# Optimization experiments

Hardware: AMD Instinct MI355X
Metric: run time of the kernel (lower is better)

## Reference

```python
import jax, jax.numpy as jnp
import numpy as np

V, D, E, S, L = 32000, 1024, 2048, 128, 4  # vocab, d_model, e=expansion*d, d_head, n_layers
B, T = 2, 2048


def _layernorm(x, g, b, eps=1e-5):
    mu = jnp.mean(x, axis=-1, keepdims=True)
    var = jnp.var(x, axis=-1, keepdims=True)
    return (x - mu) * jax.lax.rsqrt(var + eps) * g + b


def _rope_tables(t, dim):
    half = dim // 2
    inv_freq = 1.0 / (10000.0 ** (jnp.arange(0, dim, 2, dtype=jnp.float32) / dim))  # (half,)
    freqs = jnp.arange(t, dtype=jnp.float32)[:, None] * inv_freq[None, :]           # (T, half)
    return jnp.cos(freqs), jnp.sin(freqs)


def _apply_rope(x, cos, sin):
    half = x.shape[-1] // 2
    x1, x2 = x[..., :half], x[..., half:]
    return jnp.concatenate([x1 * cos - x2 * sin, x1 * sin + x2 * cos], axis=-1)


def setup_inputs() -> dict:
    key = jax.random.key(0)
    ks = jax.random.split(key, 12)
    def init(k, shape, fan_in):
        return jax.random.normal(k, shape, jnp.float32) * (fan_in ** -0.5)
    return {
        "tokens": jax.random.randint(ks[0], (B, T), 0, V, dtype=jnp.int64),
        "emb":    init(ks[1], (V, D), D),
        "Wu":     init(ks[2], (L, D, E), D),
        "Wv":     init(ks[3], (L, D, E), D),
        "Wq":     init(ks[4], (L, E, S), E),
        "Wk":     init(ks[5], (L, E, S), E),
        "Wo":     init(ks[6], (L, E, D), E),
        "ln_g":   jnp.ones((L, D), jnp.float32),
        "ln_b":   jnp.zeros((L, D), jnp.float32),
        "lnf_g":  jnp.ones((D,), jnp.float32),
        "lnf_b":  jnp.zeros((D,), jnp.float32),
        "Wlm":    init(ks[7], (D, V), D),
    }


def reference(tokens, emb, Wu, Wv, Wq, Wk, Wo, ln_g, ln_b, lnf_g, lnf_b, Wlm):
    t = tokens.shape[1]
    cos, sin = _rope_tables(t, S)                      # (T, S/2) each
    causal = jnp.tril(jnp.ones((t, t), bool))          # causal mask
    scale = 1.0 / np.sqrt(S)
    x = emb[tokens]                                    # (B, T, D)
    for i in range(L):
        xn = _layernorm(x, ln_g[i], ln_b[i])
        u = jax.nn.silu(xn @ Wu[i])                    # (B, T, E) gate branch
        v = jax.nn.silu(xn @ Wv[i])                    # (B, T, E) value branch
        q = _apply_rope(u @ Wq[i], cos, sin)           # (B, T, S)
        k = _apply_rope(v @ Wk[i], cos, sin)           # (B, T, S)
        attn = jnp.einsum('bts,bus->btu', q, k) * scale   # (B, T, T) single-head
        attn = jnp.where(causal, attn, -1e9)
        attn = jnp.square(jnp.maximum(attn, 0.0))      # relu^2 instead of softmax
        av = jnp.einsum('btu,bue->bte', attn, v)       # (B, T, E)
        x = x + (u * av) @ Wo[i]                       # gated output + residual
    x = _layernorm(x, lnf_g, lnf_b)
    return x @ Wlm                                     # (B, T, V) logits
```

## Files before the change

kernel.cpp:

```cpp
#include <hip/hip_runtime.h>
#include <math.h>


#define Bz 2
#define Tt 2048
#define Dd 1024
#define Ee 2048
#define Ss 128
#define Ll 4
#define Vv 32000
#define BT (Bz * Tt)

typedef __attribute__((ext_vector_type(8))) _Float16 f16x8;
typedef __attribute__((ext_vector_type(4))) _Float16 f16x4;
typedef __attribute__((ext_vector_type(4))) float    f32x4;

__device__ __forceinline__ void load_lds16(const void* g, void* l) {
  __builtin_amdgcn_global_load_lds(
      (const __attribute__((address_space(1))) void*)g,
      (__attribute__((address_space(3))) void*)l, 16, 0, 0);
}

#define FENCE asm volatile("" ::: "memory")
#define BARRIER do { FENCE; __builtin_amdgcn_s_barrier(); FENCE; } while (0)

enum { EPI_F32 = 0, EPI_SILU = 1, EPI_SCORES = 2, EPI_RESID = 3, EPI_GATED = 4 };

__device__ __forceinline__ int xcd_swz(int id, int nwg) {
  int q = nwg >> 3, r = nwg & 7;
  int x = id & 7, o = id >> 3;
  return (x < r ? x * (q + 1) : r * (q + 1) + (x - r) * q) + o;
}

template <int EPI>
__global__ void __launch_bounds__(512) gemm256(
    const _Float16* __restrict__ A, long sA,
    const _Float16* __restrict__ Bt, long sB,
    void* __restrict__ Cp, long sC,
    int M, int N, int K, int lda, int ldb, int ldc) {
  const int bz = blockIdx.z;
  A += (size_t)bz * sA;
  Bt += (size_t)bz * sB;

  const int nbm = M >> 8;
  const int id = xcd_swz(blockIdx.x, gridDim.x);
  const int bm = id % nbm, bn = id / nbm;
  const int row0 = bm << 8, col0 = bn << 8;

  __shared__ __align__(16) char smem[131072];
  _Float16* const Abuf0 = (_Float16*)smem;
  _Float16* const Bbuf0 = (_Float16*)(smem + 65536);

  const int tid = threadIdx.x, lane = tid & 63, w = tid >> 6;
  const int mu = w >> 2, nu = w & 3;
  const int fr = lane & 15, kg = lane >> 4;
  const int srow = (w << 3) + (lane >> 3);
  const int sg = (lane & 7) ^ ((lane >> 3) & 7);
  const _Float16* Asrc = A + (size_t)(row0 + srow) * lda + sg * 8;
  const _Float16* Bsrc = Bt + (size_t)(col0 + srow) * ldb + sg * 8;
  const int gx[2] = { ((kg) ^ (fr & 7)) << 3, ((4 + kg) ^ (fr & 7)) << 3 };

#define ST_A(BUF, KT, Q) load_lds16(Asrc + (size_t)(Q) * 64 * lda + (size_t)(KT) * 64, \
                                    (void*)&Abuf0[(BUF) * 16384 + (Q) * 4096 + (w << 9)])
#define ST_B(BUF, KT, Q) load_lds16(Bsrc + (size_t)(Q) * 64 * ldb + (size_t)(KT) * 64, \
                                    (void*)&Bbuf0[(BUF) * 16384 + (Q) * 4096 + (w << 9)])
#define RD_A(BUF, MH)                                                          \
  { _Pragma("unroll") for (int j = 0; j < 4; ++j)                              \
    _Pragma("unroll") for (int ks = 0; ks < 2; ++ks)                           \
      af[j][ks] = *(const f16x8*)&Abuf0[(BUF) * 16384 +                        \
          (mu * 128 + (MH) * 64 + j * 16 + fr) * 64 + gx[ks]]; }
#define RD_B(BUF, NH, BQ)                                                      \
  { _Pragma("unroll") for (int i = 0; i < 2; ++i)                              \
    _Pragma("unroll") for (int ks = 0; ks < 2; ++ks)                           \
      BQ[i][ks] = *(const f16x8*)&Bbuf0[(BUF) * 16384 +                        \
          (nu * 64 + (NH) * 32 + i * 16 + fr) * 64 + gx[ks]]; }
#define MFMA_Q(MH, NH, BQ)                                                     \
  { _Pragma("unroll") for (int ks = 0; ks < 2; ++ks)                           \
    _Pragma("unroll") for (int j = 0; j < 4; ++j)                              \
    _Pragma("unroll") for (int i = 0; i < 2; ++i)                              \
      acc[(MH) * 4 + j][(NH) * 2 + i] = __builtin_amdgcn_mfma_f32_16x16x32_f16( \
          af[j][ks], BQ[i][ks], acc[(MH) * 4 + j][(NH) * 2 + i], 0, 0, 0); }

  f32x4 acc[8][4];
#pragma unroll
  for (int m = 0; m < 8; ++m)
#pragma unroll
    for (int n = 0; n < 4; ++n)
#pragma unroll
      for (int e = 0; e < 4; ++e) acc[m][n][e] = 0.f;

  f16x8 af[4][2], bfA[2][2], bfB[2][2];

  const int NT = K >> 6;
  ST_B(0, 0, 0); ST_B(0, 0, 1); ST_B(0, 0, 2); ST_B(0, 0, 3);
  ST_A(0, 0, 0); ST_A(0, 0, 1); ST_A(0, 0, 2); ST_A(0, 0, 3);
  asm volatile("s_waitcnt vmcnt(0)" ::: "memory");
  BARRIER;

  for (int t = 0; t < NT; ++t) {
    const int b = t & 1, nb = b ^ 1;
    const int kn = (t + 1 < NT) ? t + 1 : t;
    RD_A(b, 0);
    RD_B(b, 0, bfA);
    RD_B(b, 1, bfB);
    ST_B(nb, kn, 0); ST_B(nb, kn, 1); ST_B(nb, kn, 2); ST_B(nb, kn, 3);
    ST_A(nb, kn, 0); ST_A(nb, kn, 1); ST_A(nb, kn, 2); ST_A(nb, kn, 3);
    asm volatile("s_waitcnt lgkmcnt(4)" ::: "memory");
    __builtin_amdgcn_sched_barrier(0);
    __builtin_amdgcn_s_setprio(1); MFMA_Q(0, 0, bfA); __builtin_amdgcn_s_setprio(0);
    asm volatile("s_waitcnt lgkmcnt(0)" ::: "memory");
    __builtin_amdgcn_sched_barrier(0);
    __builtin_amdgcn_s_setprio(1); MFMA_Q(0, 1, bfB); __builtin_amdgcn_s_setprio(0);
    RD_A(b, 1);
    asm volatile("s_waitcnt lgkmcnt(0)" ::: "memory");
    __builtin_amdgcn_sched_barrier(0);
    __builtin_amdgcn_s_setprio(1); MFMA_Q(1, 0, bfA); MFMA_Q(1, 1, bfB);
    __builtin_amdgcn_s_setprio(0);
    asm volatile("s_waitcnt vmcnt(0)" ::: "memory");
    BARRIER;
  }

  if (EPI == EPI_F32) {
    float* Cb = (float*)Cp + (size_t)bz * sC;
#pragma unroll
    for (int p = 0; p < 2; ++p) {
      __syncthreads();
      if (mu == p) {
#pragma unroll
        for (int m = 0; m < 8; ++m)
#pragma unroll
          for (int n = 0; n < 4; ++n) {
            int rl = m * 16 + (kg << 2);
            int col = nu * 64 + n * 16 + fr;
#pragma unroll
            for (int r = 0; r < 4; ++r) {
              int row = rl + r;
              *(float*)(smem + (row << 10) + ((col << 2) ^ ((row & 7) << 4))) =
                  acc[m][n][r];
            }
          }
      }
      __syncthreads();
#pragma unroll
      for (int j = 0; j < 16; ++j) {
        int row = j * 8 + w;
        f32x4 d = *(const f32x4*)(smem + (row << 10) +
                                  ((lane << 4) ^ ((row & 7) << 4)));
        *(f32x4*)&Cb[(size_t)(row0 + p * 128 + row) * ldc + col0 + (lane << 2)] = d;
      }
    }
  } else {
    _Float16* Ch = (_Float16*)Cp + (size_t)bz * sC;
    __syncthreads();
#pragma unroll
    for (int m = 0; m < 8; ++m)
#pragma unroll
      for (int n = 0; n < 4; ++n) {
        int rl = mu * 128 + m * 16 + (kg << 2);
        int col = nu * 64 + n * 16 + fr;
#pragma unroll
        for (int r = 0; r < 4; ++r) {
          int row = rl + r;
          float v = acc[m][n][r];
          *(_Float16*)(smem + (row << 9) + ((col << 1) ^ ((row & 7) << 4))) =
              (_Float16)(v / (1.f + expf(-v)));
        }
      }
    __syncthreads();
#pragma unroll
    for (int j = 0; j < 16; ++j) {
      int row = j * 16 + w * 2 + (lane >> 5);
      int g = lane & 31;
      f16x8 d = *(const f16x8*)(smem + (row << 9) +
                                ((g << 4) ^ ((row & 7) << 4)));
      *(f16x8*)&Ch[(size_t)(row0 + row) * ldc + col0 + (g << 3)] = d;
    }
  }
#undef ST_A
#undef ST_B
#undef RD_A
#undef RD_B
#undef MFMA_Q
}

#define BM 128
#define BN 128
#define BK 32

template <int EPI>
__global__ void __launch_bounds__(256, 2) gemm_bt(
    const _Float16* __restrict__ A, long sA,
    const _Float16* __restrict__ Bt, long sB,
    void* __restrict__ Cp, long sC,
    int M, int N, int K, int lda, int ldb, int ldc, int causal,
    const _Float16* __restrict__ U) {
  int bm = blockIdx.x, bn = blockIdx.y, bz = blockIdx.z;
  if (EPI == EPI_SCORES && bn > bm) return;
  A += (size_t)bz * sA;
  Bt += (size_t)bz * sB;

  int Keff = K;
  if (causal == 2) {
    int km = (bm + 1) * BM;
    Keff = km < K ? km : K;
  }

  __shared__ __align__(16) _Float16 As[BM * BK];
  __shared__ __align__(16) _Float16 Bs[BN * BK];

  int tid = threadIdx.x;
  int lane = tid & 63, wave = tid >> 6;
  int wr = (wave >> 1) << 6;
  int wc = (wave & 1) << 6;
  int row0 = bm * BM, col0 = bn * BN;
  int fr = lane & 15;
  int kg = lane >> 4;
  int srow = lane >> 2;
  int scol = (lane & 3) << 3;

  f32x4 acc[4][4];
#pragma unroll
  for (int i = 0; i < 4; i++)
#pragma unroll
    for (int j = 0; j < 4; j++)
#pragma unroll
      for (int e = 0; e < 4; e++) acc[i][j][e] = 0.f;

  const f16x8* As8 = (const f16x8*)As;
  const f16x8* Bs8 = (const f16x8*)Bs;

  for (int k0 = 0; k0 < Keff; k0 += BK) {
    __syncthreads();
#pragma unroll
    for (int i = 0; i < 2; i++) {
      int rb = (wave * 2 + i) * 16;
      load_lds16(A + (size_t)(row0 + rb + srow) * lda + k0 + scol,
                 (void*)&As[rb * BK]);
      load_lds16(Bt + (size_t)(col0 + rb + srow) * ldb + k0 + scol,
                 (void*)&Bs[rb * BK]);
    }
    asm volatile("s_waitcnt vmcnt(0)" ::: "memory");
    __syncthreads();

    f16x8 af[4], bf[4];
#pragma unroll
    for (int m = 0; m < 4; m++)
      af[m] = As8[(size_t)(wr + m * 16 + fr) * (BK / 8) + kg];
#pragma unroll
    for (int n = 0; n < 4; n++)
      bf[n] = Bs8[(size_t)(wc + n * 16 + fr) * (BK / 8) + kg];
#pragma unroll
    for (int m = 0; m < 4; m++)
#pragma unroll
      for (int n = 0; n < 4; n++)
        acc[m][n] =
            __builtin_amdgcn_mfma_f32_16x16x32_f16(af[m], bf[n], acc[m][n], 0, 0, 0);
  }

#pragma unroll
  for (int m = 0; m < 4; m++) {
    int gr0 = row0 + wr + m * 16 + (kg << 2);
#pragma unroll
    for (int n = 0; n < 4; n++) {
      int gc = col0 + wc + n * 16 + fr;
#pragma unroll
      for (int r = 0; r < 4; r++) {
        float v = acc[m][n][r];
        size_t ci = (size_t)(gr0 + r) * ldc + gc;
        if (EPI == EPI_F32) {
          ((float*)Cp + (size_t)bz * sC)[ci] = v;
        } else if (EPI == EPI_SILU) {
          ((_Float16*)Cp + (size_t)bz * sC)[ci] =
              (_Float16)(v / (1.f + expf(-v)));
        } else if (EPI == EPI_SCORES) {
          float s = v * 0.08838834764831845f;
          s = fmaxf(s, 0.f);
          s = (gc <= gr0 + r) ? s * s : 0.f;
          ((_Float16*)Cp + (size_t)bz * sC)[ci] = (_Float16)s;
        } else if (EPI == EPI_GATED) {
          const _Float16* Ub = U + (size_t)bz * sC;
          ((_Float16*)Cp + (size_t)bz * sC)[ci] = (_Float16)((float)Ub[ci] * v);
        } else {
          ((float*)Cp)[ci] += v;
        }
      }
    }
  }
}

__global__ void __launch_bounds__(256) ln_kernel(const float* __restrict__ x,
                                                 const float* __restrict__ g,
                                                 const float* __restrict__ b,
                                                 _Float16* __restrict__ out) {
  int row = blockIdx.x, tid = threadIdx.x;
  float4 v = ((const float4*)(x + (size_t)row * Dd))[tid];
  float s = v.x + v.y + v.z + v.w;
  float q = v.x * v.x + v.y * v.y + v.z * v.z + v.w * v.w;
#pragma unroll
  for (int off = 32; off > 0; off >>= 1) {
    s += __shfl_down(s, off, 64);
    q += __shfl_down(q, off, 64);
  }
  __shared__ float ss[4], sq[4];
  int lane = tid & 63, wv = tid >> 6;
  if (lane == 0) { ss[wv] = s; sq[wv] = q; }
  __syncthreads();
  s = ss[0] + ss[1] + ss[2] + ss[3];
  q = sq[0] + sq[1] + sq[2] + sq[3];
  float mu = s * (1.f / Dd);
  float var = q * (1.f / Dd) - mu * mu;
  float rs = rsqrtf(var + 1e-5f);
  float4 gg = ((const float4*)g)[tid];
  float4 bb = ((const float4*)b)[tid];
  f16x4 o;
  o[0] = (_Float16)((v.x - mu) * rs * gg.x + bb.x);
  o[1] = (_Float16)((v.y - mu) * rs * gg.y + bb.y);
  o[2] = (_Float16)((v.z - mu) * rs * gg.z + bb.z);
  o[3] = (_Float16)((v.w - mu) * rs * gg.w + bb.w);
  ((f16x4*)(out + (size_t)row * Dd))[tid] = o;
}

__global__ void embed_kernel(const int* __restrict__ toks,
                             const float* __restrict__ emb,
                             float* __restrict__ x) {
  int row = blockIdx.x, tid = threadIdx.x;
  long t = toks[row];
  ((float4*)(x + (size_t)row * Dd))[tid] =
      ((const float4*)(emb + (size_t)t * Dd))[tid];
}

__global__ void rope_table_kernel(float* __restrict__ cosT,
                                  float* __restrict__ sinT) {
  int idx = blockIdx.x * 256 + threadIdx.x;
  int t = idx >> 6, i = idx & 63;
  float inv = powf(10000.f, (float)(2 * i) * (-1.f / 128.f));
  float a = (float)t * inv;
  cosT[idx] = cosf(a);
  sinT[idx] = sinf(a);
}

__global__ void rope_kernel(const float* __restrict__ pre,
                            _Float16* __restrict__ o16,
                            const float* __restrict__ cosT,
                            const float* __restrict__ sinT) {
  int row = blockIdx.x * 4 + threadIdx.y;
  int i = threadIdx.x;
  int z = blockIdx.y;
  const float* p = pre + (size_t)z * BT * Ss + (size_t)row * Ss;
  _Float16* o = o16 + (size_t)z * BT * Ss + (size_t)row * Ss;
  int t = row & (Tt - 1);
  float c = cosT[t * 64 + i], sn = sinT[t * 64 + i];
  float x1 = p[i], x2 = p[i + 64];
  o[i] = (_Float16)(x1 * c - x2 * sn);
  o[i + 64] = (_Float16)(x1 * sn + x2 * c);
}

template <typename TIn>
__global__ void transconv_kernel(const TIn* __restrict__ in,
                                 _Float16* __restrict__ out, int R, int C,
                                 long s_in, long s_out) {
  __shared__ float tile[64][65];
  in += (size_t)blockIdx.z * s_in;
  out += (size_t)blockIdx.z * s_out;
  int r0 = blockIdx.y * 64, c0 = blockIdx.x * 64;
  int tx = threadIdx.x & 63, ty = threadIdx.x >> 6;
#pragma unroll
  for (int p = 0; p < 16; p++) {
    int r = p * 4 + ty;
    tile[r][tx] = (float)in[(size_t)(r0 + r) * C + c0 + tx];
  }
  __syncthreads();
#pragma unroll
  for (int p = 0; p < 16; p++) {
    int r = p * 4 + ty;
    out[(size_t)(c0 + r) * R + r0 + tx] = (_Float16)tile[tx][r];
  }
}

extern "C" void kernel_launch(void* const* d_in, const int* in_sizes, int n_in,
                              void* d_out, int out_size, void* d_ws,
                              size_t ws_size, hipStream_t stream) {
  const int*   tokens = (const int*)d_in[0];
  const float* emb    = (const float*)d_in[1];
  const float* Wu     = (const float*)d_in[2];
  const float* Wv     = (const float*)d_in[3];
  const float* Wq     = (const float*)d_in[4];
  const float* Wk     = (const float*)d_in[5];
  const float* Wo     = (const float*)d_in[6];
  const float* ln_g   = (const float*)d_in[7];
  const float* ln_b   = (const float*)d_in[8];
  const float* lnf_g  = (const float*)d_in[9];
  const float* lnf_b  = (const float*)d_in[10];
  const float* Wlm    = (const float*)d_in[11];
  float* out = (float*)d_out;
  (void)in_sizes; (void)n_in; (void)out_size;

  char* wsp = (char*)d_ws;
  size_t off = 0;
  auto alloc = [&](size_t bytes) -> void* {
    void* p = wsp + off;
    off = (off + bytes + 255) & ~(size_t)255;
    return p;
  };

  float*    x     = (float*)alloc((size_t)BT * Dd * 4);
  _Float16* xn    = (_Float16*)alloc((size_t)BT * Dd * 2);
  _Float16* uvh   = (_Float16*)alloc((size_t)2 * BT * Ee * 2);
  _Float16* vT    = (_Float16*)alloc((size_t)Bz * Ee * Tt * 2);
  float*    qkpre = (float*)alloc((size_t)2 * BT * Ss * 4);
  _Float16* qkh   = (_Float16*)alloc((size_t)2 * BT * Ss * 2);
  _Float16* attn  = (_Float16*)alloc((size_t)Bz * Tt * Tt * 2);
  _Float16* gh    = (_Float16*)alloc((size_t)BT * Ee * 2);
  float*    cosT  = (float*)alloc((size_t)Tt * 64 * 4);
  float*    sinT  = (float*)alloc((size_t)Tt * 64 * 4);
  _Float16* WuvT  = (_Float16*)alloc((size_t)2 * Ll * Ee * Dd * 2);
  _Float16* WqkT  = (_Float16*)alloc((size_t)2 * Ll * Ss * Ee * 2);
  _Float16* WoT   = (_Float16*)alloc((size_t)Ll * Dd * Ee * 2);
  _Float16* WlmT  = (_Float16*)alloc((size_t)Vv * Dd * 2);
  if (off > ws_size) return;

  transconv_kernel<float><<<dim3(Ee / 64, Dd / 64, Ll), 256, 0, stream>>>(
      Wu, WuvT, Dd, Ee, (long)Dd * Ee, (long)Ee * Dd);
  transconv_kernel<float><<<dim3(Ee / 64, Dd / 64, Ll), 256, 0, stream>>>(
      Wv, WuvT + (size_t)Ll * Ee * Dd, Dd, Ee, (long)Dd * Ee, (long)Ee * Dd);
  transconv_kernel<float><<<dim3(Ss / 64, Ee / 64, Ll), 256, 0, stream>>>(
      Wq, WqkT, Ee, Ss, (long)Ee * Ss, (long)Ss * Ee);
  transconv_kernel<float><<<dim3(Ss / 64, Ee / 64, Ll), 256, 0, stream>>>(
      Wk, WqkT + (size_t)Ll * Ss * Ee, Ee, Ss, (long)Ee * Ss, (long)Ss * Ee);
  transconv_kernel<float><<<dim3(Dd / 64, Ee / 64, Ll), 256, 0, stream>>>(
      Wo, WoT, Ee, Dd, (long)Ee * Dd, (long)Dd * Ee);
  transconv_kernel<float><<<dim3(Vv / 64, Dd / 64, 1), 256, 0, stream>>>(
      Wlm, WlmT, Dd, Vv, 0, 0);

  rope_table_kernel<<<(Tt * 64) / 256, 256, 0, stream>>>(cosT, sinT);
  embed_kernel<<<BT, 256, 0, stream>>>(tokens, emb, x);

  for (int l = 0; l < Ll; l++) {
    ln_kernel<<<BT, 256, 0, stream>>>(x, ln_g + (size_t)l * Dd,
                                      ln_b + (size_t)l * Dd, xn);
    gemm256<EPI_SILU><<<dim3((BT / 256) * (Ee / 256), 1, 2), 512, 0, stream>>>(
        xn, 0, WuvT + (size_t)l * Ee * Dd, (long)Ll * Ee * Dd, (void*)uvh,
        (long)BT * Ee, BT, Ee, Dd, Dd, Dd, Ee);
    gemm_bt<EPI_F32><<<dim3(BT / BM, Ss / BN, 2), 256, 0, stream>>>(
        uvh, (long)BT * Ee, WqkT + (size_t)l * Ss * Ee, (long)Ll * Ss * Ee,
        (void*)qkpre, (long)BT * Ss, BT, Ss, Ee, Ee, Ee, Ss, 0, nullptr);
    rope_kernel<<<dim3(BT / 4, 2), dim3(64, 4), 0, stream>>>(qkpre, qkh, cosT,
                                                             sinT);
    transconv_kernel<_Float16><<<dim3(Ee / 64, Tt / 64, Bz), 256, 0, stream>>>(
        uvh + (size_t)BT * Ee, vT, Tt, Ee, (long)Tt * Ee, (long)Ee * Tt);
    gemm_bt<EPI_SCORES><<<dim3(Tt / BM, Tt / BN, Bz), 256, 0, stream>>>(
        qkh, (long)Tt * Ss, qkh + (size_t)BT * Ss, (long)Tt * Ss, (void*)attn,
        (long)Tt * Tt, Tt, Tt, Ss, Ss, Ss, Tt, 0, nullptr);
    gemm_bt<EPI_GATED><<<dim3(Tt / BM, Ee / BN, Bz), 256, 0, stream>>>(
        attn, (long)Tt * Tt, vT, (long)Ee * Tt, (void*)gh, (long)Tt * Ee, Tt,
        Ee, Tt, Tt, Tt, Ee, 2, uvh);
    gemm_bt<EPI_RESID><<<dim3(BT / BM, Dd / BN, 1), 256, 0, stream>>>(
        gh, 0, WoT + (size_t)l * Dd * Ee, 0, (void*)x, 0, BT, Dd, Ee, Ee, Ee,
        Dd, 0, nullptr);
  }

  ln_kernel<<<BT, 256, 0, stream>>>(x, lnf_g, lnf_b, xn);
  gemm256<EPI_F32><<<dim3((BT / 256) * (Vv / 256), 1, 1), 512, 0, stream>>>(
      xn, 0, WlmT, 0, (void*)out, 0, BT, Vv, Dd, Dd, Dd, Vv);
}
```

Before: 1.345 ms.

## Shrink gemm256 tile to 256x128 with BK=32 for higher occupancy

The large GEMM kernel (used for the Wu/Wv projection and the LM head) drops from a 256x256 tile with BK=64 and 128KB of LDS to a 256x128 tile with BK=32 and 48KB of LDS. Launch bounds now request 4 blocks, and the grid doubles. The per-k-step schedule becomes a single batch of 16 MFMAs after all fragment loads, and both epilogues are rewritten for the smaller staging buffer. The aim is more resident waves to hide latency. In exchange, each tile reuses less data, barriers run twice as often per K, and the finer interleaved MFMA/LDS schedule is lost.

Result: slower. 1.389 ms (+3.3%).

```diff
diff --git a/kernel.cpp b/kernel.cpp
--- a/kernel.cpp
+++ b/kernel.cpp
@@ -33,7 +33,7 @@
 }
 
 template <int EPI>
-__global__ void __launch_bounds__(512) gemm256(
+__global__ void __launch_bounds__(512, 4) gemm256(
     const _Float16* __restrict__ A, long sA,
     const _Float16* __restrict__ Bt, long sB,
     void* __restrict__ Cp, long sC,
@@ -45,76 +45,60 @@
   const int nbm = M >> 8;
   const int id = xcd_swz(blockIdx.x, gridDim.x);
   const int bm = id % nbm, bn = id / nbm;
-  const int row0 = bm << 8, col0 = bn << 8;
-
-  __shared__ __align__(16) char smem[131072];
-  _Float16* const Abuf0 = (_Float16*)smem;
-  _Float16* const Bbuf0 = (_Float16*)(smem + 65536);
+  const int row0 = bm << 8, col0 = bn << 7;
+
+  __shared__ __align__(16) char smem[49152];
+  _Float16* const Ab = (_Float16*)smem;
+  _Float16* const Bb = (_Float16*)(smem + 32768);
 
   const int tid = threadIdx.x, lane = tid & 63, w = tid >> 6;
-  const int mu = w >> 2, nu = w & 3;
+  const int mu = w >> 1, nu = w & 1;
   const int fr = lane & 15, kg = lane >> 4;
-  const int srow = (w << 3) + (lane >> 3);
-  const int sg = (lane & 7) ^ ((lane >> 3) & 7);
+  const int srow = w * 16 + (lane >> 2);
+  const int sg = (lane & 3) ^ ((lane >> 2) & 3);
   const _Float16* Asrc = A + (size_t)(row0 + srow) * lda + sg * 8;
   const _Float16* Bsrc = Bt + (size_t)(col0 + srow) * ldb + sg * 8;
-  const int gx[2] = { ((kg) ^ (fr & 7)) << 3, ((4 + kg) ^ (fr & 7)) << 3 };
-
-#define ST_A(BUF, KT, Q) load_lds16(Asrc + (size_t)(Q) * 64 * lda + (size_t)(KT) * 64, \
-                                    (void*)&Abuf0[(BUF) * 16384 + (Q) * 4096 + (w << 9)])
-#define ST_B(BUF, KT, Q) load_lds16(Bsrc + (size_t)(Q) * 64 * ldb + (size_t)(KT) * 64, \
-                                    (void*)&Bbuf0[(BUF) * 16384 + (Q) * 4096 + (w << 9)])
-#define RD_A(BUF, MH)                                                          \
-  { _Pragma("unroll") for (int j = 0; j < 4; ++j)                              \
-    _Pragma("unroll") for (int ks = 0; ks < 2; ++ks)                           \
-      af[j][ks] = *(const f16x8*)&Abuf0[(BUF) * 16384 +                        \
-          (mu * 128 + (MH) * 64 + j * 16 + fr) * 64 + gx[ks]]; }
-#define RD_B(BUF, NH, BQ)                                                      \
-  { _Pragma("unroll") for (int i = 0; i < 2; ++i)                              \
-    _Pragma("unroll") for (int ks = 0; ks < 2; ++ks)                           \
-      BQ[i][ks] = *(const f16x8*)&Bbuf0[(BUF) * 16384 +                        \
-          (nu * 64 + (NH) * 32 + i * 16 + fr) * 64 + gx[ks]]; }
-#define MFMA_Q(MH, NH, BQ)                                                     \
-  { _Pragma("unroll") for (int ks = 0; ks < 2; ++ks)                           \
-    _Pragma("unroll") for (int j = 0; j < 4; ++j)                              \
-    _Pragma("unroll") for (int i = 0; i < 2; ++i)                              \
-      acc[(MH) * 4 + j][(NH) * 2 + i] = __builtin_amdgcn_mfma_f32_16x16x32_f16( \
-          af[j][ks], BQ[i][ks], acc[(MH) * 4 + j][(NH) * 2 + i], 0, 0, 0); }
-
-  f32x4 acc[8][4];
-#pragma unroll
-  for (int m = 0; m < 8; ++m)
+  const int gA = ((kg ^ (fr & 3)) << 3);
+
+#define ST_A(BUF, KT, Q) load_lds16(Asrc + (size_t)(Q) * 128 * lda + (size_t)(KT) * 32, \
+                                    (void*)&Ab[(BUF) * 8192 + (Q) * 4096 + w * 512])
+#define ST_B(BUF, KT)    load_lds16(Bsrc + (size_t)(KT) * 32, \
+                                    (void*)&Bb[(BUF) * 4096 + w * 512])
+
+  f32x4 acc[4][4];
+#pragma unroll
+  for (int m = 0; m < 4; ++m)
 #pragma unroll
     for (int n = 0; n < 4; ++n)
 #pragma unroll
       for (int e = 0; e < 4; ++e) acc[m][n][e] = 0.f;
 
-  f16x8 af[4][2], bfA[2][2], bfB[2][2];
-
-  const int NT = K >> 6;
-  ST_B(0, 0, 0); ST_B(0, 0, 1); ST_B(0, 0, 2); ST_B(0, 0, 3);
-  ST_A(0, 0, 0); ST_A(0, 0, 1); ST_A(0, 0, 2); ST_A(0, 0, 3);
+  f16x8 af[4], bf[4];
+
+  const int NT = K >> 5;
+  ST_A(0, 0, 0); ST_A(0, 0, 1); ST_B(0, 0);
   asm volatile("s_waitcnt vmcnt(0)" ::: "memory");
   BARRIER;
 
   for (int t = 0; t < NT; ++t) {
     const int b = t & 1, nb = b ^ 1;
     const int kn = (t + 1 < NT) ? t + 1 : t;
-    RD_A(b, 0);
-    RD_B(b, 0, bfA);
-    RD_B(b, 1, bfB);
-    ST_B(nb, kn, 0); ST_B(nb, kn, 1); ST_B(nb, kn, 2); ST_B(nb, kn, 3);
-    ST_A(nb, kn, 0); ST_A(nb, kn, 1); ST_A(nb, kn, 2); ST_A(nb, kn, 3);
-    asm volatile("s_waitcnt lgkmcnt(4)" ::: "memory");
-    __builtin_amdgcn_sched_barrier(0);
-    __builtin_amdgcn_s_setprio(1); MFMA_Q(0, 0, bfA); __builtin_amdgcn_s_setprio(0);
+    ST_A(nb, kn, 0); ST_A(nb, kn, 1); ST_B(nb, kn);
+#pragma unroll
+    for (int m = 0; m < 4; ++m)
+      af[m] = *(const f16x8*)&Ab[b * 8192 + (mu * 64 + m * 16 + fr) * 32 + gA];
+#pragma unroll
+    for (int n = 0; n < 4; ++n)
+      bf[n] = *(const f16x8*)&Bb[b * 4096 + (nu * 64 + n * 16 + fr) * 32 + gA];
     asm volatile("s_waitcnt lgkmcnt(0)" ::: "memory");
     __builtin_amdgcn_sched_barrier(0);
-    __builtin_amdgcn_s_setprio(1); MFMA_Q(0, 1, bfB); __builtin_amdgcn_s_setprio(0);
-    RD_A(b, 1);
-    asm volatile("s_waitcnt lgkmcnt(0)" ::: "memory");
-    __builtin_amdgcn_sched_barrier(0);
-    __builtin_amdgcn_s_setprio(1); MFMA_Q(1, 0, bfA); MFMA_Q(1, 1, bfB);
+    __builtin_amdgcn_s_setprio(1);
+#pragma unroll
+    for (int m = 0; m < 4; ++m)
+#pragma unroll
+      for (int n = 0; n < 4; ++n)
+        acc[m][n] =
+            __builtin_amdgcn_mfma_f32_16x16x32_f16(af[m], bf[n], acc[m][n], 0, 0, 0);
     __builtin_amdgcn_s_setprio(0);
     asm volatile("s_waitcnt vmcnt(0)" ::: "memory");
     BARRIER;
@@ -123,64 +107,65 @@
   if (EPI == EPI_F32) {
     float* Cb = (float*)Cp + (size_t)bz * sC;
 #pragma unroll
-    for (int p = 0; p < 2; ++p) {
+    for (int p = 0; p < 4; ++p) {
       __syncthreads();
       if (mu == p) {
 #pragma unroll
-        for (int m = 0; m < 8; ++m)
+        for (int m = 0; m < 4; ++m)
 #pragma unroll
           for (int n = 0; n < 4; ++n) {
-            int rl = m * 16 + (kg << 2);
             int col = nu * 64 + n * 16 + fr;
 #pragma unroll
             for (int r = 0; r < 4; ++r) {
-              int row = rl + r;
-              *(float*)(smem + (row << 10) + ((col << 2) ^ ((row & 7) << 4))) =
+              int row = m * 16 + (kg << 2) + r;
+              *(float*)(smem + (row << 9) + ((col << 2) ^ ((row & 7) << 4))) =
                   acc[m][n][r];
             }
           }
       }
       __syncthreads();
 #pragma unroll
-      for (int j = 0; j < 16; ++j) {
-        int row = j * 8 + w;
-        f32x4 d = *(const f32x4*)(smem + (row << 10) +
-                                  ((lane << 4) ^ ((row & 7) << 4)));
-        *(f32x4*)&Cb[(size_t)(row0 + p * 128 + row) * ldc + col0 + (lane << 2)] = d;
+      for (int rr = 0; rr < 4; ++rr) {
+        int row = rr * 16 + w * 2 + (lane >> 5);
+        f32x4 d = *(const f32x4*)(smem + (row << 9) +
+                                  (((lane & 31) << 4) ^ ((row & 7) << 4)));
+        *(f32x4*)&Cb[(size_t)(row0 + p * 64 + row) * ldc + col0 +
+                     ((lane & 31) << 2)] = d;
       }
     }
   } else {
     _Float16* Ch = (_Float16*)Cp + (size_t)bz * sC;
-    __syncthreads();
-#pragma unroll
-    for (int m = 0; m < 8; ++m)
-#pragma unroll
-      for (int n = 0; n < 4; ++n) {
-        int rl = mu * 128 + m * 16 + (kg << 2);
-        int col = nu * 64 + n * 16 + fr;
-#pragma unroll
-        for (int r = 0; r < 4; ++r) {
-          int row = rl + r;
-          float v = acc[m][n][r];
-          *(_Float16*)(smem + (row << 9) + ((col << 1) ^ ((row & 7) << 4))) =
-              (_Float16)(v / (1.f + expf(-v)));
-        }
+#pragma unroll
+    for (int p = 0; p < 2; ++p) {
+      __syncthreads();
+      if ((mu >> 1) == p) {
+#pragma unroll
+        for (int m = 0; m < 4; ++m)
+#pragma unroll
+          for (int n = 0; n < 4; ++n) {
+            int col = nu * 64 + n * 16 + fr;
+#pragma unroll
+            for (int r = 0; r < 4; ++r) {
+              int row = (mu & 1) * 64 + m * 16 + (kg << 2) + r;
+              float v = acc[m][n][r];
+              *(_Float16*)(smem + (row << 8) + ((col << 1) ^ ((row & 7) << 4))) =
+                  (_Float16)(v / (1.f + expf(-v)));
+            }
+          }
       }
-    __syncthreads();
-#pragma unroll
-    for (int j = 0; j < 16; ++j) {
-      int row = j * 16 + w * 2 + (lane >> 5);
-      int g = lane & 31;
-      f16x8 d = *(const f16x8*)(smem + (row << 9) +
-                                ((g << 4) ^ ((row & 7) << 4)));
-      *(f16x8*)&Ch[(size_t)(row0 + row) * ldc + col0 + (g << 3)] = d;
+      __syncthreads();
+#pragma unroll
+      for (int rr = 0; rr < 4; ++rr) {
+        int row = rr * 32 + w * 4 + (lane >> 4);
+        f16x8 d = *(const f16x8*)(smem + (row << 8) +
+                                  (((lane & 15) << 4) ^ ((row & 7) << 4)));
+        *(f16x8*)&Ch[(size_t)(row0 + p * 128 + row) * ldc + col0 +
+                     ((lane & 15) << 3)] = d;
+      }
     }
   }
 #undef ST_A
 #undef ST_B
-#undef RD_A
-#undef RD_B
-#undef MFMA_Q
 }
 
 #define BM 128
@@ -438,7 +423,7 @@
   for (int l = 0; l < Ll; l++) {
     ln_kernel<<<BT, 256, 0, stream>>>(x, ln_g + (size_t)l * Dd,
                                       ln_b + (size_t)l * Dd, xn);
-    gemm256<EPI_SILU><<<dim3((BT / 256) * (Ee / 256), 1, 2), 512, 0, stream>>>(
+    gemm256<EPI_SILU><<<dim3((BT / 256) * (Ee / 128), 1, 2), 512, 0, stream>>>(
         xn, 0, WuvT + (size_t)l * Ee * Dd, (long)Ll * Ee * Dd, (void*)uvh,
         (long)BT * Ee, BT, Ee, Dd, Dd, Dd, Ee);
     gemm_bt<EPI_F32><<<dim3(BT / BM, Ss / BN, 2), 256, 0, stream>>>(
@@ -460,6 +445,6 @@
   }
 
   ln_kernel<<<BT, 256, 0, stream>>>(x, lnf_g, lnf_b, xn);
-  gemm256<EPI_F32><<<dim3((BT / 256) * (Vv / 256), 1, 1), 512, 0, stream>>>(
+  gemm256<EPI_F32><<<dim3((BT / 256) * (Vv / 128), 1, 1), 512, 0, stream>>>(
       xn, 0, WlmT, 0, (void*)out, 0, BT, Vv, Dd, Dd, Dd, Vv);
 }
```
